# Kernel optimization log

Measured on AMD Instinct MI355X. Metric: run time of the kernel, lower is better.

Reference implementation:

```python
import jax, jax.numpy as jnp
import numpy as np

NUM_EMBED = 1024
EMBED_DIM = 256
DECAY = 0.99
EPS = 1e-05
COMMIT = 0.25


def setup_inputs() -> dict:
    key = jax.random.key(0)
    k1, k2, k3 = jax.random.split(key, 3)
    z = jax.random.normal(k1, (64, 32, 32, EMBED_DIM), dtype=jnp.float32)
    lim = 1.0 / NUM_EMBED
    embeddings = jax.random.uniform(k2, (NUM_EMBED, EMBED_DIM), minval=-lim, maxval=lim, dtype=jnp.float32)
    ema_embed = jax.random.uniform(k3, (NUM_EMBED, EMBED_DIM), minval=-lim, maxval=lim, dtype=jnp.float32)
    cluster_size = jnp.zeros((NUM_EMBED,), dtype=jnp.float32)
    return {"z": z, "embeddings": embeddings, "ema_embed": ema_embed, "cluster_size": cluster_size}


def reference(z, embeddings, ema_embed, cluster_size):
    B, H, W, D = z.shape
    zf = z.reshape(-1, D)  # [N, D]
    # squared euclidean distances to codebook: [N, K]
    distances = (zf ** 2).sum(-1, keepdims=True) + (embeddings ** 2).sum(-1) - 2.0 * (zf @ embeddings.T)
    closest = jnp.argmin(distances, axis=-1)  # [N] int
    quantized_indices = closest.reshape(B, H, W)[:, None]  # [B,1,H,W]
    quantized = embeddings[closest].reshape(z.shape)  # gather instead of one-hot GEMM

    # --- training-mode EMA codebook update (buffer math, no grads) ---
    n_i = jnp.zeros((NUM_EMBED,), dtype=zf.dtype).at[closest].add(1.0)  # per-code counts
    new_cluster = cluster_size * DECAY + n_i * (1.0 - DECAY)
    dw = jnp.zeros_like(embeddings).at[closest].add(zf)  # scatter-add of assigned vectors
    new_ema = ema_embed * DECAY + dw * (1.0 - DECAY)
    n = new_cluster.sum()
    new_cluster = (new_cluster + EPS) / (n + NUM_EMBED * EPS) * n
    new_embeddings = new_ema / new_cluster[:, None]

    commitment_loss = jnp.mean((quantized - z) ** 2)
    st_quantized = z + jax.lax.stop_gradient(quantized - z)  # straight-through
    loss = commitment_loss * COMMIT
    return loss, st_quantized, quantized_indices, new_embeddings, new_cluster, new_ema
```

## Files before the change

kernel.cpp:

```cpp
#include <hip/hip_runtime.h>
#include <float.h>
#include <stdint.h>

#define K_EMB 1024
#define D_EMB 256

typedef _Float16 half8 __attribute__((ext_vector_type(8)));
typedef float f32x4_t __attribute__((ext_vector_type(4)));

typedef const __attribute__((address_space(1))) void* as1cv;
typedef __attribute__((address_space(3))) void* as3v;


__global__ void convert_e_kernel(const float* __restrict__ e, _Float16* __restrict__ ehp,
                                 float* __restrict__ t2, unsigned int* __restrict__ flag_cnt) {
  if (blockIdx.x == 0 && threadIdx.x == 0) { flag_cnt[0] = 0; flag_cnt[1] = 0; }
  int row = blockIdx.x * 4 + (threadIdx.x >> 6);
  int lane = threadIdx.x & 63;
  float4 v = ((const float4*)(e + (size_t)row * D_EMB))[lane];
  float s = v.x * v.x + v.y * v.y + v.z * v.z + v.w * v.w;
#pragma unroll
  for (int off = 32; off > 0; off >>= 1) s += __shfl_down(s, off, 64);
  if (lane == 0) t2[row] = s;
  _Float16* dst = ehp + (size_t)row * D_EMB + lane * 4;
  dst[0] = (_Float16)v.x; dst[1] = (_Float16)v.y;
  dst[2] = (_Float16)v.z; dst[3] = (_Float16)v.w;
}


#define BM 128
#define CCH 32
#define NCH (K_EMB / CCH)
#define DELTA 1.5e-4f

__launch_bounds__(256, 3)
__global__ void argmin_mfma_kernel(const float* __restrict__ z,
                                   const _Float16* __restrict__ eh,
                                   const float* __restrict__ t2,
                                   int* __restrict__ closest,
                                   float* __restrict__ idx_out,
                                   unsigned int* __restrict__ flag_cnt,
                                   unsigned int* __restrict__ flag_row,
                                   unsigned int* __restrict__ flag_cand,
                                   unsigned int* __restrict__ flag2) {
  __shared__ _Float16 ebuf[4][CCH * D_EMB];
  const int tid = threadIdx.x;
  const int wid = tid >> 6;
  const int lane = tid & 63;
  const int c = lane & 15, g = lane >> 4;
  const int row0 = blockIdx.x * BM + wid * 32;

  half8 A[2][8];
#pragma unroll
  for (int fr = 0; fr < 2; ++fr)
#pragma unroll
    for (int df = 0; df < 8; ++df) {
      const float* zp = z + (size_t)(row0 + fr * 16 + c) * D_EMB + df * 32 + g * 8;
      const float4 v0 = *(const float4*)zp;
      const float4 v1 = *(const float4*)(zp + 4);
      half8 h;
      h[0] = (_Float16)v0.x; h[1] = (_Float16)v0.y; h[2] = (_Float16)v0.z; h[3] = (_Float16)v0.w;
      h[4] = (_Float16)v1.x; h[5] = (_Float16)v1.y; h[6] = (_Float16)v1.z; h[7] = (_Float16)v1.w;
      A[fr][df] = h;
    }

  float m1[8], m2[8], m3[8];
  int k1[8], k2[8];
#pragma unroll
  for (int s = 0; s < 8; ++s) { m1[s] = FLT_MAX; m2[s] = FLT_MAX; m3[s] = FLT_MAX; k1[s] = 0; k2[s] = 0; }

#define INS(s, dvv, kkv)                                        \
  {                                                             \
    const float dv_ = (dvv); const int kk_ = (kkv);             \
    const bool lt1 = dv_ < m1[s];                               \
    const bool lt2 = dv_ < m2[s];                               \
    m3[s] = __builtin_amdgcn_fmed3f(m2[s], m3[s], dv_);         \
    const float nm2 = __builtin_amdgcn_fmed3f(m1[s], m2[s], dv_); \
    k2[s] = lt1 ? k1[s] : (lt2 ? kk_ : k2[s]);                  \
    m2[s] = nm2;                                                \
    m1[s] = fminf(m1[s], dv_);                                  \
    k1[s] = lt1 ? kk_ : k1[s];                                  \
  }

  const int rswz = (c & 7) << 3;

  int sgs[4];
#pragma unroll
  for (int u = 0; u < 4; ++u) {
    const int gidx = (wid * 4 + u) * 64 + lane;
    sgs[u] = (gidx & ~7) | ((gidx & 7) ^ ((gidx >> 5) & 7));
  }

#define ISSUE(cbn, buf)                                                              \
  {                                                                                  \
    const _Float16* src_ = eh + (size_t)(cbn) * (CCH * D_EMB);                       \
    _Float16* db_ = &ebuf[buf][0];                                                   \
    _Pragma("unroll")                                                                \
    for (int u = 0; u < 4; ++u)                                                      \
      __builtin_amdgcn_global_load_lds((as1cv)(src_ + (size_t)sgs[u] * 8),           \
                                       (as3v)(db_ + (wid * 4 + u) * 512), 16, 0, 0); \
  }

#define MFMA_CHUNK(rb_, ACC)                                                         \
  {                                                                                  \
    _Pragma("unroll")                                                                \
    for (int fr = 0; fr < 2; ++fr)                                                   \
      _Pragma("unroll")                                                              \
      for (int fc = 0; fc < 2; ++fc) ACC[fr][fc] = (f32x4_t){0.f, 0.f, 0.f, 0.f};    \
    _Pragma("unroll")                                                                \
    for (int d = 0; d < 8; ++d) {                                                    \
      half8 Bh[2];                                                                   \
      _Pragma("unroll")                                                              \
      for (int fc = 0; fc < 2; ++fc) {                                               \
        const int elem = (d * 32 + g * 8) ^ rswz;                                    \
        Bh[fc] = *(const half8*)(&ebuf[rb_][(fc * 16 + c) * D_EMB + elem]);          \
      }                                                                              \
      _Pragma("unroll")                                                              \
      for (int fr = 0; fr < 2; ++fr)                                                 \
        _Pragma("unroll")                                                            \
        for (int fc = 0; fc < 2; ++fc)                                               \
          ACC[fr][fc] = __builtin_amdgcn_mfma_f32_16x16x32_f16(A[fr][d], Bh[fc],     \
                                                               ACC[fr][fc], 0, 0, 0);\
    }                                                                                \
  }

#define FOLD(ACC, cb_)                                                               \
  {                                                                                  \
    _Pragma("unroll")                                                                \
    for (int fc = 0; fc < 2; ++fc) {                                                 \
      const int kk = (cb_)*CCH + fc * 16 + c;                                        \
      const float t2c = t2[kk];                                                      \
      _Pragma("unroll")                                                              \
      for (int fr = 0; fr < 2; ++fr)                                                 \
        _Pragma("unroll")                                                            \
        for (int r = 0; r < 4; ++r) {                                                \
          const float dv = fmaf(-2.f, ACC[fr][fc][r], t2c);                          \
          const int s = fr * 4 + r;                                                  \
          INS(s, dv, kk)                                                             \
        }                                                                            \
    }                                                                                \
  }

  f32x4_t accA[2][2], accB[2][2];

  ISSUE(0, 0)
  ISSUE(1, 1)

  for (int cb = 0; cb < NCH - 2; cb += 2) {
    asm volatile("s_waitcnt vmcnt(4)" ::: "memory");
    __builtin_amdgcn_s_barrier();
    __builtin_amdgcn_sched_barrier(0);
    ISSUE(cb + 2, (cb + 2) & 3)
    MFMA_CHUNK(cb & 3, accA)
    if (cb) FOLD(accB, cb - 1)
    asm volatile("s_waitcnt vmcnt(4)" ::: "memory");
    __builtin_amdgcn_s_barrier();
    __builtin_amdgcn_sched_barrier(0);
    ISSUE(cb + 3, (cb + 3) & 3)
    MFMA_CHUNK((cb + 1) & 3, accB)
    FOLD(accA, cb)
  }
  asm volatile("s_waitcnt vmcnt(4)" ::: "memory");
  __builtin_amdgcn_s_barrier();
  __builtin_amdgcn_sched_barrier(0);
  MFMA_CHUNK((NCH - 2) & 3, accA)
  FOLD(accB, NCH - 3)
  asm volatile("s_waitcnt vmcnt(0)" ::: "memory");
  __builtin_amdgcn_s_barrier();
  __builtin_amdgcn_sched_barrier(0);
  MFMA_CHUNK((NCH - 1) & 3, accB)
  FOLD(accA, NCH - 2)
  FOLD(accB, NCH - 1)
#undef MFMA_CHUNK
#undef FOLD
#undef ISSUE

#pragma unroll
  for (int m = 1; m <= 8; m <<= 1) {
#pragma unroll
    for (int s = 0; s < 8; ++s) {
      const float om1 = __shfl_xor(m1[s], m, 64);
      const int ok1 = __shfl_xor(k1[s], m, 64);
      const float om2 = __shfl_xor(m2[s], m, 64);
      const int ok2 = __shfl_xor(k2[s], m, 64);
      const float om3 = __shfl_xor(m3[s], m, 64);
      INS(s, om1, ok1)
      INS(s, om2, ok2)
      m3[s] = fminf(m3[s], om3);
    }
  }
#undef INS

  if (c == 0) {
#pragma unroll
    for (int s = 0; s < 8; ++s) {
      const int fr = s >> 2, r = s & 3;
      const int row = row0 + fr * 16 + g * 4 + r;
      closest[row] = k1[s];
      idx_out[row] = (float)k1[s];
      if (m2[s] - m1[s] < DELTA) {
        if (m3[s] - m1[s] < DELTA) {
          const unsigned int p = atomicAdd(&flag_cnt[1], 1u);
          flag2[p] = (unsigned int)row;
        } else {
          const unsigned int p = atomicAdd(&flag_cnt[0], 1u);
          flag_row[p] = (unsigned int)row;
          flag_cand[p] = (unsigned int)k1[s] | ((unsigned int)k2[s] << 10);
        }
      }
    }
  }
}


__launch_bounds__(256, 4)
__global__ void fixup_kernel(const float* __restrict__ z, const float* __restrict__ emb,
                             const float* __restrict__ t2,
                             const unsigned int* __restrict__ flag_cnt,
                             const unsigned int* __restrict__ flag1_row,
                             const unsigned int* __restrict__ flag1_cand,
                             const unsigned int* __restrict__ flag2,
                             int* __restrict__ closest, float* __restrict__ idx_out) {
  const int tid = threadIdx.x;
  {
    const int q = tid & 3;
    const unsigned int cnt = flag_cnt[0];
    const unsigned int nquads = (gridDim.x * 256) >> 2;
    for (unsigned int i = (blockIdx.x * 256 + tid) >> 2; i < cnt; i += nquads) {
      const int row = (int)flag1_row[i];
      const unsigned int cand = flag1_cand[i];
      const int ka = (int)(cand & 1023u), kb = (int)((cand >> 10) & 1023u);
      const float4* zp = (const float4*)(z + (size_t)row * D_EMB) + q * 16;
      const float4* ap = (const float4*)(emb + (size_t)ka * D_EMB) + q * 16;
      const float4* bp = (const float4*)(emb + (size_t)kb * D_EMB) + q * 16;
      float s0 = 0.f, sa = 0.f, sb = 0.f;
#pragma unroll 8
      for (int u = 0; u < 16; ++u) {
        const float4 zv = zp[u], av = ap[u], bv = bp[u];
        s0 = fmaf(zv.x, zv.x, s0); s0 = fmaf(zv.y, zv.y, s0);
        s0 = fmaf(zv.z, zv.z, s0); s0 = fmaf(zv.w, zv.w, s0);
        sa = fmaf(zv.x, av.x, sa); sa = fmaf(zv.y, av.y, sa);
        sa = fmaf(zv.z, av.z, sa); sa = fmaf(zv.w, av.w, sa);
        sb = fmaf(zv.x, bv.x, sb); sb = fmaf(zv.y, bv.y, sb);
        sb = fmaf(zv.z, bv.z, sb); sb = fmaf(zv.w, bv.w, sb);
      }
#pragma unroll
      for (int m = 1; m <= 2; m <<= 1) {
        s0 += __shfl_xor(s0, m, 64);
        sa += __shfl_xor(sa, m, 64);
        sb += __shfl_xor(sb, m, 64);
      }
      if (q == 0) {
        const float da = (s0 + t2[ka]) - 2.f * sa;
        const float db = (s0 + t2[kb]) - 2.f * sb;
        int kbest = ka;
        if (db < da || (db == da && kb < ka)) kbest = kb;
        closest[row] = kbest;
        idx_out[row] = (float)kbest;
      }
    }
  }
  __shared__ float zs[D_EMB];
  __shared__ float t1s;
  __shared__ float redm[4];
  __shared__ int redk[4];
  const int lane = tid & 63, wv = tid >> 6;
  const unsigned int cnt2 = flag_cnt[1];
  for (unsigned int j = blockIdx.x; j < cnt2; j += gridDim.x) {
    __syncthreads();
    const int row = (int)flag2[j];
    if (wv == 0) {
      const float4 v = ((const float4*)(z + (size_t)row * D_EMB))[lane];
      ((float4*)zs)[lane] = v;
      float s = v.x * v.x + v.y * v.y + v.z * v.z + v.w * v.w;
#pragma unroll
      for (int off = 32; off > 0; off >>= 1) s += __shfl_down(s, off, 64);
      if (lane == 0) t1s = s;
    }
    __syncthreads();
    const float4* e0 = (const float4*)(emb + (size_t)(4 * tid + 0) * D_EMB);
    const float4* e1 = (const float4*)(emb + (size_t)(4 * tid + 1) * D_EMB);
    const float4* e2 = (const float4*)(emb + (size_t)(4 * tid + 2) * D_EMB);
    const float4* e3 = (const float4*)(emb + (size_t)(4 * tid + 3) * D_EMB);
    const float4* zp4 = (const float4*)zs;
    float a0 = 0.f, a1 = 0.f, a2 = 0.f, a3 = 0.f;
    for (int i = 0; i < 64; ++i) {
      const float4 z4 = zp4[i];
      const float4 v0 = e0[i], v1 = e1[i], v2 = e2[i], v3 = e3[i];
      a0 = fmaf(z4.x, v0.x, a0); a0 = fmaf(z4.y, v0.y, a0);
      a0 = fmaf(z4.z, v0.z, a0); a0 = fmaf(z4.w, v0.w, a0);
      a1 = fmaf(z4.x, v1.x, a1); a1 = fmaf(z4.y, v1.y, a1);
      a1 = fmaf(z4.z, v1.z, a1); a1 = fmaf(z4.w, v1.w, a1);
      a2 = fmaf(z4.x, v2.x, a2); a2 = fmaf(z4.y, v2.y, a2);
      a2 = fmaf(z4.z, v2.z, a2); a2 = fmaf(z4.w, v2.w, a2);
      a3 = fmaf(z4.x, v3.x, a3); a3 = fmaf(z4.y, v3.y, a3);
      a3 = fmaf(z4.z, v3.z, a3); a3 = fmaf(z4.w, v3.w, a3);
    }
    const float t1v = t1s;
    float best = FLT_MAX;
    int bk = 0x7fffffff;
    const float dvs[4] = {(t1v + t2[4 * tid + 0]) - 2.f * a0,
                          (t1v + t2[4 * tid + 1]) - 2.f * a1,
                          (t1v + t2[4 * tid + 2]) - 2.f * a2,
                          (t1v + t2[4 * tid + 3]) - 2.f * a3};
#pragma unroll
    for (int cc = 0; cc < 4; ++cc) {
      const int k = 4 * tid + cc;
      if (dvs[cc] < best) { best = dvs[cc]; bk = k; }
    }
#pragma unroll
    for (int m = 1; m <= 32; m <<= 1) {
      const float ob = __shfl_xor(best, m, 64);
      const int ok = __shfl_xor(bk, m, 64);
      if (ob < best || (ob == best && ok < bk)) { best = ob; bk = ok; }
    }
    if (lane == 0) { redm[wv] = best; redk[wv] = bk; }
    __syncthreads();
    if (tid == 0) {
      float b = redm[0];
      int k = redk[0];
#pragma unroll
      for (int w = 1; w < 4; ++w)
        if (redm[w] < b || (redm[w] == b && redk[w] < k)) { b = redm[w]; k = redk[w]; }
      closest[row] = k;
      idx_out[row] = (float)k;
    }
  }
}


__global__ void hist1_kernel(const int* __restrict__ closest, unsigned int* __restrict__ rank,
                             unsigned int* __restrict__ blockhist) {
  __shared__ unsigned int lh[K_EMB];
  const int t = threadIdx.x;
  lh[t] = 0;
  __syncthreads();
  const int row = blockIdx.x * 1024 + t;
  rank[row] = atomicAdd(&lh[closest[row]], 1u);
  __syncthreads();
  blockhist[blockIdx.x * K_EMB + t] = lh[t];
}

__global__ void hist2_kernel(unsigned int* __restrict__ blockhist, const float* __restrict__ cs,
                             unsigned int* __restrict__ base, float* __restrict__ newc,
                             float* __restrict__ o_ncl, int nblocks) {
  __shared__ unsigned int sc[K_EMB];
  __shared__ float fr[K_EMB];
  const int bin = threadIdx.x;
  unsigned int s = 0;
  if (nblocks == 64) {
    unsigned int v[64];
#pragma unroll
    for (int b = 0; b < 64; ++b) v[b] = blockhist[b * K_EMB + bin];
#pragma unroll
    for (int b = 0; b < 64; ++b) { const unsigned int t = v[b]; blockhist[b * K_EMB + bin] = s; s += t; }
  } else {
    for (int b = 0; b < nblocks; ++b) {
      const unsigned int v = blockhist[b * K_EMB + bin];
      blockhist[b * K_EMB + bin] = s;
      s += v;
    }
  }
  sc[bin] = s;
  __syncthreads();
  for (int off = 1; off < K_EMB; off <<= 1) {
    const unsigned int t = (bin >= off) ? sc[bin - off] : 0u;
    __syncthreads();
    sc[bin] += t;
    __syncthreads();
  }
  base[bin] = sc[bin] - s;
  const float pre = cs[bin] * 0.99f + (float)s * (float)(1.0 - 0.99);
  fr[bin] = pre;
  __syncthreads();
  for (int st = 512; st > 0; st >>= 1) {
    if (bin < st) fr[bin] += fr[bin + st];
    __syncthreads();
  }
  const float n = fr[0];
  const float ncl = (pre + 1e-5f) / (n + (float)(K_EMB * 1e-5)) * n;
  newc[bin] = ncl;
  o_ncl[bin] = ncl;
}

__global__ void hist3_kernel(const int* __restrict__ closest, const unsigned int* __restrict__ rank,
                             const unsigned int* __restrict__ blockhist,
                             const unsigned int* __restrict__ base,
                             unsigned int* __restrict__ sorted) {
  const int t = threadIdx.x;
  const int row = blockIdx.x * 1024 + t;
  const int k = closest[row];
  sorted[base[k] + blockhist[blockIdx.x * K_EMB + k] + rank[row]] = (unsigned int)row;
}


__global__ void dwsum_kernel(const float* __restrict__ z, const unsigned int* __restrict__ sorted,
                             const unsigned int* __restrict__ base, const float* __restrict__ ema,
                             const float* __restrict__ newc, const float* __restrict__ emb,
                             float* __restrict__ o_st, float* __restrict__ o_nema,
                             float* __restrict__ o_nemb, float* __restrict__ loss_part, int N) {
  const int k = blockIdx.x;
  const int lane = threadIdx.x & 63, wv = threadIdx.x >> 6;
  const unsigned int b0 = base[k];
  const unsigned int b1 = (k == K_EMB - 1) ? (unsigned int)N : base[k + 1];
  const float4 ev = ((const float4*)(emb + (size_t)k * D_EMB))[lane];
  float4 acc = {0.f, 0.f, 0.f, 0.f};
  float ls = 0.f;
  for (unsigned int j = b0 + wv; j < b1; j += 4) {
    const unsigned int row = sorted[j];
    const float4 zv = ((const float4*)(z + (size_t)row * D_EMB))[lane];
    const float dx = ev.x - zv.x, dy = ev.y - zv.y, dz = ev.z - zv.z, dww = ev.w - zv.w;
    float* sp = o_st + (size_t)row * D_EMB + lane * 4;
    sp[0] = zv.x + dx; sp[1] = zv.y + dy; sp[2] = zv.z + dz; sp[3] = zv.w + dww;
    ls = fmaf(dx, dx, ls); ls = fmaf(dy, dy, ls);
    ls = fmaf(dz, dz, ls); ls = fmaf(dww, dww, ls);
    acc.x += zv.x; acc.y += zv.y; acc.z += zv.z; acc.w += zv.w;
  }
  __shared__ float4 red[256];
  __shared__ float lred[256];
  red[threadIdx.x] = acc;
  lred[threadIdx.x] = ls;
  __syncthreads();
  for (int s = 128; s > 0; s >>= 1) {
    if (threadIdx.x < s) lred[threadIdx.x] += lred[threadIdx.x + s];
    __syncthreads();
  }
  if (threadIdx.x == 0) loss_part[k] = lred[0];
  if (wv == 0) {
    const float4 a1 = red[64 + lane], a2 = red[128 + lane], a3 = red[192 + lane];
    acc = red[lane];
    acc.x += a1.x + a2.x + a3.x;
    acc.y += a1.y + a2.y + a3.y;
    acc.z += a1.z + a2.z + a3.z;
    acc.w += a1.w + a2.w + a3.w;
    const float4 emv = ((const float4*)ema)[k * 64 + lane];
    const float nc = newc[k];
    const int off = k * D_EMB + lane * 4;
    float ne;
    ne = emv.x * 0.99f + acc.x * (float)(1.0 - 0.99); o_nema[off + 0] = ne; o_nemb[off + 0] = ne / nc;
    ne = emv.y * 0.99f + acc.y * (float)(1.0 - 0.99); o_nema[off + 1] = ne; o_nemb[off + 1] = ne / nc;
    ne = emv.z * 0.99f + acc.z * (float)(1.0 - 0.99); o_nema[off + 2] = ne; o_nemb[off + 2] = ne / nc;
    ne = emv.w * 0.99f + acc.w * (float)(1.0 - 0.99); o_nema[off + 3] = ne; o_nemb[off + 3] = ne / nc;
  }
}

__global__ void loss_final_kernel(const float* __restrict__ loss_part,
                                  float* __restrict__ o_loss, int nrows) {
  const int i = threadIdx.x;
  __shared__ double dred[1024];
  dred[i] = (double)loss_part[i];
  __syncthreads();
  for (int s = 512; s > 0; s >>= 1) {
    if (i < s) dred[i] += dred[i + s];
    __syncthreads();
  }
  if (i == 0) o_loss[0] = (float)(0.25 * (dred[0] / ((double)nrows * (double)D_EMB)));
}


extern "C" void kernel_launch(void* const* d_in, const int* in_sizes, int n_in,
                              void* d_out, int out_size, void* d_ws, size_t ws_size,
                              hipStream_t stream) {
  const float* z = (const float*)d_in[0];
  const float* emb = (const float*)d_in[1];
  const float* ema = (const float*)d_in[2];
  const float* cs = (const float*)d_in[3];
  const int N = in_sizes[0] / D_EMB;
  const int NB = N / 1024;

  float* out = (float*)d_out;
  float* o_loss = out;
  float* o_st = out + 1;
  float* o_idx = o_st + (size_t)N * D_EMB;
  float* o_nemb = o_idx + N;
  float* o_ncl = o_nemb + (size_t)K_EMB * D_EMB;
  float* o_nema = o_ncl + K_EMB;

  float* ws = (float*)d_ws;
  float* t2 = ws;
  float* newc = t2 + K_EMB;
  float* loss_part = newc + K_EMB;
  unsigned int* flag_cnt = (unsigned int*)(loss_part + K_EMB);
  unsigned int* basep = flag_cnt + 4;
  _Float16* ehp = (_Float16*)(basep + K_EMB);
  int* closest = (int*)(ehp + (size_t)K_EMB * D_EMB);
  unsigned int* flag_row = (unsigned int*)(closest + N);
  unsigned int* flag_cand = flag_row + N;
  unsigned int* sorted = flag_cand + N;
  unsigned int* flag2 = sorted + N;

  unsigned int* rank = flag_row;
  unsigned int* blockhist = flag_cand;

  convert_e_kernel<<<K_EMB / 4, 256, 0, stream>>>(emb, ehp, t2, flag_cnt);
  argmin_mfma_kernel<<<N / BM, 256, 0, stream>>>(z, ehp, t2, closest, o_idx,
                                                 flag_cnt, flag_row, flag_cand, flag2);
  fixup_kernel<<<256, 256, 0, stream>>>(z, emb, t2, flag_cnt, flag_row, flag_cand, flag2,
                                        closest, o_idx);
  hist1_kernel<<<NB, 1024, 0, stream>>>(closest, rank, blockhist);
  hist2_kernel<<<1, 1024, 0, stream>>>(blockhist, cs, basep, newc, o_ncl, NB);
  hist3_kernel<<<NB, 1024, 0, stream>>>(closest, rank, blockhist, basep, sorted);
  dwsum_kernel<<<K_EMB, 256, 0, stream>>>(z, sorted, basep, ema, newc, emb,
                                          o_st, o_nema, o_nemb, loss_part, N);
  loss_final_kernel<<<1, 1024, 0, stream>>>(loss_part, o_loss, N);
}
```

Measured before the change: 179.7 us.

## Restructure argmin MFMA pipeline to triple-buffered single-chunk loop with sched groups

Replaces the two-way unrolled loop with a single-chunk loop over a triple-buffered LDS ring. The old loop had separate accumulators so the fold of one chunk could overlap the MFMAs of the next; the new loop keeps one accumulator set per chunk. Each chunk now loads all B fragments from LDS up front, runs the MFMAs, then folds, with sched_group_barrier hints to interleave LDS reads and MFMAs. Launch bounds drop from 3 to 2 blocks per CU, which gives more registers for the hoisted fragments at the cost of occupancy, and the loss of cross-chunk fold/MFMA overlap may expose latency.

Result: no change. 180.1 us (+0.2%).

```diff
diff --git a/kernel.cpp b/kernel.cpp
--- a/kernel.cpp
+++ b/kernel.cpp
@@ -33,7 +33,7 @@
 #define NCH (K_EMB / CCH)
 #define DELTA 1.5e-4f
 
-__launch_bounds__(256, 3)
+__launch_bounds__(256, 2)
 __global__ void argmin_mfma_kernel(const float* __restrict__ z,
                                    const _Float16* __restrict__ eh,
                                    const float* __restrict__ t2,
@@ -43,7 +43,7 @@
                                    unsigned int* __restrict__ flag_row,
                                    unsigned int* __restrict__ flag_cand,
                                    unsigned int* __restrict__ flag2) {
-  __shared__ _Float16 ebuf[4][CCH * D_EMB];
+  __shared__ _Float16 ebuf[3][CCH * D_EMB];
   const int tid = threadIdx.x;
   const int wid = tid >> 6;
   const int lane = tid & 63;
@@ -101,31 +101,32 @@
                                        (as3v)(db_ + (wid * 4 + u) * 512), 16, 0, 0); \
   }
 
-#define MFMA_CHUNK(rb_, ACC)                                                         \
+#define COMPUTE(rb_, cb_)                                                            \
   {                                                                                  \
+    half8 Bh[2][8];                                                                  \
+    _Pragma("unroll")                                                                \
+    for (int fc = 0; fc < 2; ++fc)                                                   \
+      _Pragma("unroll")                                                              \
+      for (int d = 0; d < 8; ++d) {                                                  \
+        const int elem = (d * 32 + g * 8) ^ rswz;                                    \
+        Bh[fc][d] = *(const half8*)(&ebuf[rb_][(fc * 16 + c) * D_EMB + elem]);       \
+      }                                                                              \
+    f32x4_t acc[2][2];                                                               \
     _Pragma("unroll")                                                                \
     for (int fr = 0; fr < 2; ++fr)                                                   \
       _Pragma("unroll")                                                              \
-      for (int fc = 0; fc < 2; ++fc) ACC[fr][fc] = (f32x4_t){0.f, 0.f, 0.f, 0.f};    \
+      for (int fc = 0; fc < 2; ++fc) acc[fr][fc] = (f32x4_t){0.f, 0.f, 0.f, 0.f};    \
     _Pragma("unroll")                                                                \
-    for (int d = 0; d < 8; ++d) {                                                    \
-      half8 Bh[2];                                                                   \
-      _Pragma("unroll")                                                              \
-      for (int fc = 0; fc < 2; ++fc) {                                               \
-        const int elem = (d * 32 + g * 8) ^ rswz;                                    \
-        Bh[fc] = *(const half8*)(&ebuf[rb_][(fc * 16 + c) * D_EMB + elem]);          \
-      }                                                                              \
+    for (int d = 0; d < 8; ++d)                                                      \
       _Pragma("unroll")                                                              \
       for (int fr = 0; fr < 2; ++fr)                                                 \
         _Pragma("unroll")                                                            \
         for (int fc = 0; fc < 2; ++fc)                                               \
-          ACC[fr][fc] = __builtin_amdgcn_mfma_f32_16x16x32_f16(A[fr][d], Bh[fc],     \
-                                                               ACC[fr][fc], 0, 0, 0);\
-    }                                                                                \
-  }
-
-#define FOLD(ACC, cb_)                                                               \
-  {                                                                                  \
+          acc[fr][fc] = __builtin_amdgcn_mfma_f32_16x16x32_f16(A[fr][d], Bh[fc][d],  \
+                                                               acc[fr][fc], 0, 0, 0);\
+    __builtin_amdgcn_sched_group_barrier(0x010, 4, 0);        \
+    __builtin_amdgcn_sched_group_barrier(0x100, 16, 0);        \
+    __builtin_amdgcn_sched_group_barrier(0x008, 16, 0);                 \
     _Pragma("unroll")                                                                \
     for (int fc = 0; fc < 2; ++fc) {                                                 \
       const int kk = (cb_)*CCH + fc * 16 + c;                                        \
@@ -134,45 +135,32 @@
       for (int fr = 0; fr < 2; ++fr)                                                 \
         _Pragma("unroll")                                                            \
         for (int r = 0; r < 4; ++r) {                                                \
-          const float dv = fmaf(-2.f, ACC[fr][fc][r], t2c);                          \
+          const float dv = fmaf(-2.f, acc[fr][fc][r], t2c);                          \
           const int s = fr * 4 + r;                                                  \
           INS(s, dv, kk)                                                             \
         }                                                                            \
     }                                                                                \
   }
 
-  f32x4_t accA[2][2], accB[2][2];
-
   ISSUE(0, 0)
   ISSUE(1, 1)
 
-  for (int cb = 0; cb < NCH - 2; cb += 2) {
+  for (int cb = 0; cb < NCH - 1; ++cb) {
     asm volatile("s_waitcnt vmcnt(4)" ::: "memory");
     __builtin_amdgcn_s_barrier();
     __builtin_amdgcn_sched_barrier(0);
-    ISSUE(cb + 2, (cb + 2) & 3)
-    MFMA_CHUNK(cb & 3, accA)
-    if (cb) FOLD(accB, cb - 1)
-    asm volatile("s_waitcnt vmcnt(4)" ::: "memory");
-    __builtin_amdgcn_s_barrier();
-    __builtin_amdgcn_sched_barrier(0);
-    ISSUE(cb + 3, (cb + 3) & 3)
-    MFMA_CHUNK((cb + 1) & 3, accB)
-    FOLD(accA, cb)
-  }
-  asm volatile("s_waitcnt vmcnt(4)" ::: "memory");
-  __builtin_amdgcn_s_barrier();
-  __builtin_amdgcn_sched_barrier(0);
-  MFMA_CHUNK((NCH - 2) & 3, accA)
-  FOLD(accB, NCH - 3)
+    if (cb + 2 < NCH) ISSUE(cb + 2, (cb + 2) % 3)
+    const int rb = cb % 3;
+    COMPUTE(rb, cb)
+  }
   asm volatile("s_waitcnt vmcnt(0)" ::: "memory");
   __builtin_amdgcn_s_barrier();
   __builtin_amdgcn_sched_barrier(0);
-  MFMA_CHUNK((NCH - 1) & 3, accB)
-  FOLD(accA, NCH - 2)
-  FOLD(accB, NCH - 1)
-#undef MFMA_CHUNK
-#undef FOLD
+  {
+    const int rb = (NCH - 1) % 3;
+    COMPUTE(rb, NCH - 1)
+  }
+#undef COMPUTE
 #undef ISSUE
 
 #pragma unroll
```
